# Kernel tuning notes

Hardware: AMD Instinct MI355X
Metric: run time of the kernel (lower is better)

Reference implementation:

```python
import jax, jax.numpy as jnp
import numpy as np

B, G, H, C = 2, 3072, 5, 2  # batch, genes (input_size), heads, classes
EPS = 1e-6


def setup_inputs() -> dict:
    key = jax.random.key(0)
    ks = jax.random.split(key, 11)
    xav = np.sqrt(2.0 / (G + 1)).astype(np.float32)  # xavier_normal for (G,1) slices
    inp = {"x": jax.random.normal(ks[0], (B, G), jnp.float32)}
    names = ["WQ1", "WK1", "WV1", "WQ2", "WK2", "WV2", "WQ3", "WK3", "WV3"]
    for i, name in enumerate(names):
        inp[name] = jax.random.normal(ks[1 + i], (H, G), jnp.float32) * xav
    inp["W0_1"] = jnp.full((H,), 0.001, jnp.float32)
    inp["W0_2"] = jnp.full((H,), 0.001, jnp.float32)
    inp["W0_3"] = jnp.full((H,), 0.001, jnp.float32)
    inp["ln_a"] = jnp.ones((G,), jnp.float32)
    inp["ln_b"] = jnp.zeros((G,), jnp.float32)
    inp["fc_w"] = jax.random.normal(ks[10], (C, G), jnp.float32) * np.sqrt(1.0 / G).astype(np.float32)
    inp["fc_b"] = jnp.zeros((C,), jnp.float32)
    return inp


def _multihead_attn(x, WQ, WK, WV, W0):
    # x: (B,G); WQ/WK/WV: (H,G); W0: (H,)
    # per head: scores[b,i,j] = (x[b,i]*WQ[h,i]) * (x[b,j]*WK[h,j])
    # z = softmax_j(scores); zero diagonal (mask AFTER softmax, no renorm);
    # out[b,i] = sum_j z[b,i,j] * (x[b,j]*WV[h,j])
    mask = 1.0 - jnp.eye(G, dtype=x.dtype)
    outs = []
    for h in range(H):  # small structural loop over heads (checkpointed loop in torch)
        q = x * WQ[h]                                   # (B,G)
        k = x * WK[h]                                   # (B,G)
        v = x * WV[h]                                   # (B,G)
        scores = q[:, :, None] * k[:, None, :]          # (B,G,G)
        z = jax.nn.softmax(scores, axis=2) * mask       # (B,G,G)
        outs.append(jnp.einsum('bij,bj->bi', z, v))     # (B,G)
    out_h = jnp.stack(outs, axis=-1)                    # (B,G,H)
    return jnp.einsum('bgh,h->bg', out_h, W0)


def _layernorm(x, a, b):
    # torch layernorm clone: unbiased std (ddof=1), eps added to std (not var)
    mean = jnp.mean(x, axis=-1, keepdims=True)
    std = jnp.std(x, axis=-1, keepdims=True, ddof=1)
    return a * (x - mean) / (std + EPS) + b


def reference(x, WQ1, WK1, WV1, WQ2, WK2, WV2, WQ3, WK3, WV3,
              W0_1, W0_2, W0_3, ln_a, ln_b, fc_w, fc_b):
    o1 = _multihead_attn(x, WQ1, WK1, WV1, W0_1)
    h1 = x + _layernorm(o1, ln_a, ln_b)      # res_connect (dropout=identity, eval)
    o2 = _multihead_attn(h1, WQ2, WK2, WV2, W0_2)
    h2 = h1 + _layernorm(o2, ln_a, ln_b)
    o3 = _multihead_attn(h2, WQ3, WK3, WV3, W0_3)
    h3 = h2 + _layernorm(o3, ln_a, ln_b)
    # act_fun='linear' -> identity; final classifier head
    return h3 @ fc_w.T + fc_b                # (B, C)
```

## Files before the change

kernel.cpp:

```cpp
#include <hip/hip_runtime.h>
#include <math.h>

typedef float v2f __attribute__((ext_vector_type(2)));

constexpr int Gn = 3072;
constexpr int Hn = 5;
constexpr float EPSf = 1e-6f;
constexpr float L2E  = 1.4426950408889634f;

__constant__ float INVFL[5] = {
  1.0f, 0.6931471805599453f, 0.2402265069591007f,
  0.05550410866482158f, 0.009618129107628477f };

struct __align__(16) Smem {
  float hbuf[Gn];
  float coeff[Hn * 16];
  float part[15][10];
  v2f   red2[16];
};

__device__ __forceinline__ v2f mk2(float a, float b){ v2f r; r.x = a; r.y = b; return r; }
__device__ __forceinline__ v2f pk_mul(v2f a, v2f b){
  v2f d; asm("v_pk_mul_f32 %0, %1, %2" : "=v"(d) : "v"(a), "v"(b)); return d; }
__device__ __forceinline__ v2f pk_add(v2f a, v2f b){
  v2f d; asm("v_pk_add_f32 %0, %1, %2" : "=v"(d) : "v"(a), "v"(b)); return d; }
__device__ __forceinline__ v2f pk_fma(v2f a, v2f b, v2f c){
  v2f d; asm("v_pk_fma_f32 %0, %1, %2, %3" : "=v"(d) : "v"(a), "v"(b), "v"(c)); return d; }

__device__ __forceinline__ float wave_red(float v) {
  int x;
  x = __builtin_amdgcn_update_dpp(0, __float_as_int(v), 0xB1,  0xF, 0xF, true);
  v += __int_as_float(x);
  x = __builtin_amdgcn_update_dpp(0, __float_as_int(v), 0x4E,  0xF, 0xF, true);
  v += __int_as_float(x);
  x = __builtin_amdgcn_update_dpp(0, __float_as_int(v), 0x141, 0xF, 0xF, true);
  v += __int_as_float(x);
  x = __builtin_amdgcn_update_dpp(0, __float_as_int(v), 0x140, 0xF, 0xF, true);
  v += __int_as_float(x);
  v += __shfl_xor(v, 16, 64);
  v += __shfl_xor(v, 32, 64);
  return v;
}

__device__ void layer(const float* __restrict__ WQ, const float* __restrict__ WK,
                      const float* __restrict__ WV, const float* __restrict__ W0,
                      const float* lnar, const float* lnbr, Smem& sm, int t)
{
  const int w = t >> 6, lane = t & 63;

  if (w < 15) {
    const int h = w / 3, sl = w % 3;
    const float4* xb4 = reinterpret_cast<const float4*>(sm.hbuf) + sl * 256;
    const float4* wk4 = reinterpret_cast<const float4*>(WK + h * Gn) + sl * 256;
    const float4* wv4 = reinterpret_cast<const float4*>(WV + h * Gn) + sl * 256;

    float4 xv[4], kk[4], vv[4];
#pragma unroll
    for (int it = 0; it < 4; ++it) {
      xv[it] = xb4[it * 64 + lane];
      kk[it] = wk4[it * 64 + lane];
      vv[it] = wv4[it * 64 + lane];
    }

    v2f N1 = mk2(0,0), N2 = N1, N3 = N1, N4 = N1;
    v2f M0 = N1, M1 = N1, M2 = N1, M3 = N1, M4 = N1;
    auto accp = [&](v2f x, v2f wkv, v2f wvv) {
      v2f k = pk_mul(x, wkv), v = pk_mul(x, wvv);
      v2f p2 = pk_mul(k, k), p3 = pk_mul(p2, k), p4 = pk_mul(p2, p2);
      N1 = pk_add(N1, k); N2 = pk_add(N2, p2); N3 = pk_add(N3, p3); N4 = pk_add(N4, p4);
      M0 = pk_add(M0, v);
      M1 = pk_fma(k,  v, M1); M2 = pk_fma(p2, v, M2);
      M3 = pk_fma(p3, v, M3); M4 = pk_fma(p4, v, M4);
    };
#pragma unroll
    for (int it = 0; it < 4; ++it) {
      accp(mk2(xv[it].x, xv[it].y), mk2(kk[it].x, kk[it].y), mk2(vv[it].x, vv[it].y));
      accp(mk2(xv[it].z, xv[it].w), mk2(kk[it].z, kk[it].w), mk2(vv[it].z, vv[it].w));
    }

    float r[9];
    r[0] = wave_red(N1.x + N1.y); r[1] = wave_red(N2.x + N2.y);
    r[2] = wave_red(N3.x + N3.y); r[3] = wave_red(N4.x + N4.y);
    r[4] = wave_red(M0.x + M0.y); r[5] = wave_red(M1.x + M1.y);
    r[6] = wave_red(M2.x + M2.y); r[7] = wave_red(M3.x + M3.y);
    r[8] = wave_red(M4.x + M4.y);
    if (lane == 0) {
#pragma unroll
      for (int m = 0; m < 9; ++m) sm.part[w][m] = r[m];
    }
  }
  __syncthreads();

  if (t < 45) {
    const int h = t / 9, r = t % 9;
    const float s = sm.part[h*3+0][r] + sm.part[h*3+1][r] + sm.part[h*3+2][r];
    const int m   = (r < 4) ? (r + 1) : (r - 4);
    const int dst = (r < 4) ? (r + 1) : (8 + (r - 4));
    sm.coeff[h*16 + dst] = s * INVFL[m];
  } else if (t < 50) {
    sm.coeff[(t - 45) * 16] = (float)Gn;
  }
  __syncthreads();

  const float xx0 = sm.hbuf[t], xx1 = sm.hbuf[t+1024], xx2 = sm.hbuf[t+2048];

  float w0r[Hn];
#pragma unroll
  for (int h = 0; h < Hn; ++h) w0r[h] = W0[h];

  float qc0,qc1,qc2, kc0,kc1,kc2, vc0,vc1,vc2;
  {
    const float* wq = WQ + t; const float* wk = WK + t; const float* wv = WV + t;
    qc0 = wq[0]; qc1 = wq[1024]; qc2 = wq[2048];
    kc0 = wk[0]; kc1 = wk[1024]; kc2 = wk[2048];
    vc0 = wv[0]; vc1 = wv[1024]; vc2 = wv[2048];
  }

  v2f o01 = mk2(0.f, 0.f);
  float o2a = 0.f;
#pragma unroll
  for (int h = 0; h < Hn; ++h) {
    float qn0,qn1,qn2, kn0,kn1,kn2, vn0,vn1,vn2;
    if (h < Hn - 1) {
      const float* wq = WQ + (h+1)*Gn + t;
      const float* wk = WK + (h+1)*Gn + t;
      const float* wv = WV + (h+1)*Gn + t;
      qn0 = wq[0]; qn1 = wq[1024]; qn2 = wq[2048];
      kn0 = wk[0]; kn1 = wk[1024]; kn2 = wk[2048];
      vn0 = wv[0]; vn1 = wv[1024]; vn2 = wv[2048];
    }
    const float4 zA = *reinterpret_cast<const float4*>(&sm.coeff[h*16]);
    const float  z4 = sm.coeff[h*16 + 4];
    const float4 fA = *reinterpret_cast<const float4*>(&sm.coeff[h*16 + 8]);
    const float  f4 = sm.coeff[h*16 + 12];
    const float  w0 = w0r[h];

    const v2f X  = mk2(xx0, xx1);
    const v2f qe = pk_mul(pk_mul(X, mk2(qc0, qc1)), mk2(L2E, L2E));
    const v2f kp = pk_mul(X, mk2(kc0, kc1));
    const v2f vp = pk_mul(X, mk2(vc0, vc1));
    v2f Z = mk2(z4, z4);
    Z = pk_fma(Z, qe, mk2(zA.w, zA.w)); Z = pk_fma(Z, qe, mk2(zA.z, zA.z));
    Z = pk_fma(Z, qe, mk2(zA.y, zA.y)); Z = pk_fma(Z, qe, mk2(zA.x, zA.x));
    v2f F = mk2(f4, f4);
    F = pk_fma(F, qe, mk2(fA.w, fA.w)); F = pk_fma(F, qe, mk2(fA.z, fA.z));
    F = pk_fma(F, qe, mk2(fA.y, fA.y)); F = pk_fma(F, qe, mk2(fA.x, fA.x));
    const v2f qk = pk_mul(qe, kp);
    const float Ex = __builtin_amdgcn_exp2f(qk.x), Ey = __builtin_amdgcn_exp2f(qk.y);
    const float rx = fmaf(-Ex, vp.x, F.x) * __builtin_amdgcn_rcpf(Z.x);
    const float ry = fmaf(-Ey, vp.y, F.y) * __builtin_amdgcn_rcpf(Z.y);
    o01 = pk_fma(mk2(w0, w0), mk2(rx, ry), o01);

    const float qe2 = xx2 * qc2 * L2E, k2 = xx2 * kc2, vv2 = xx2 * vc2;
    float Zs = z4;
    Zs = fmaf(Zs, qe2, zA.w); Zs = fmaf(Zs, qe2, zA.z);
    Zs = fmaf(Zs, qe2, zA.y); Zs = fmaf(Zs, qe2, zA.x);
    float Fs = f4;
    Fs = fmaf(Fs, qe2, fA.w); Fs = fmaf(Fs, qe2, fA.z);
    Fs = fmaf(Fs, qe2, fA.y); Fs = fmaf(Fs, qe2, fA.x);
    const float Es = __builtin_amdgcn_exp2f(qe2 * k2);
    o2a = fmaf(w0, fmaf(-Es, vv2, Fs) * __builtin_amdgcn_rcpf(Zs), o2a);

    if (h < Hn - 1) {
      qc0=qn0; qc1=qn1; qc2=qn2; kc0=kn0; kc1=kn1; kc2=kn2; vc0=vn0; vc1=vn1; vc2=vn2;
    }
  }

  float s1 = o01.x + o01.y + o2a;
  float s2 = fmaf(o01.x, o01.x, fmaf(o01.y, o01.y, o2a * o2a));
  s1 = wave_red(s1); s2 = wave_red(s2);
  if (lane == 0) sm.red2[w] = mk2(s1, s2);
  __syncthreads();
  v2f acc = sm.red2[0];
#pragma unroll
  for (int k = 1; k < 16; ++k) acc = pk_add(acc, sm.red2[k]);
  const float mean = acc.x * (1.f / (float)Gn);
  const float var  = fmaxf((acc.y - acc.x * mean) * (1.f / (float)(Gn - 1)), 0.f);
  const float inv  = __builtin_amdgcn_rcpf(sqrtf(var) + EPSf);
  sm.hbuf[t]      = xx0 + lnar[0] * (o01.x - mean) * inv + lnbr[0];
  sm.hbuf[t+1024] = xx1 + lnar[1] * (o01.y - mean) * inv + lnbr[1];
  sm.hbuf[t+2048] = xx2 + lnar[2] * (o2a   - mean) * inv + lnbr[2];
  __syncthreads();
}

__global__ __launch_bounds__(1024, 4) void net_kernel(
    const float* __restrict__ x,
    const float* __restrict__ WQ1, const float* __restrict__ WK1, const float* __restrict__ WV1,
    const float* __restrict__ WQ2, const float* __restrict__ WK2, const float* __restrict__ WV2,
    const float* __restrict__ WQ3, const float* __restrict__ WK3, const float* __restrict__ WV3,
    const float* __restrict__ W01, const float* __restrict__ W02, const float* __restrict__ W03,
    const float* __restrict__ lna, const float* __restrict__ lnb,
    const float* __restrict__ fcw, const float* __restrict__ fcb,
    float* __restrict__ out)
{
  __shared__ Smem sm;
  const int b = blockIdx.x;
  const int t = threadIdx.x;

  float lnar[3], lnbr[3];
#pragma unroll
  for (int rep = 0; rep < 3; ++rep) {
    const int i = rep * 1024 + t;
    sm.hbuf[i] = x[b * Gn + i];
    lnar[rep] = lna[i];
    lnbr[rep] = lnb[i];
  }
  __syncthreads();

  layer(WQ1, WK1, WV1, W01, lnar, lnbr, sm, t);
  layer(WQ2, WK2, WV2, W02, lnar, lnbr, sm, t);
  layer(WQ3, WK3, WV3, W03, lnar, lnbr, sm, t);

  v2f sacc = mk2(0.f, 0.f);
#pragma unroll
  for (int rep = 0; rep < 3; ++rep) {
    const int i = rep * 1024 + t;
    const float hv = sm.hbuf[i];
    sacc = pk_fma(mk2(hv, hv), mk2(fcw[i], fcw[Gn + i]), sacc);
  }
  const float s0 = wave_red(sacc.x), s1 = wave_red(sacc.y);
  const int w = t >> 6, lane = t & 63;
  if (lane == 0) sm.red2[w] = mk2(s0, s1);
  __syncthreads();
  if (t == 0) {
    v2f acc = sm.red2[0];
#pragma unroll
    for (int k = 1; k < 16; ++k) acc = pk_add(acc, sm.red2[k]);
    out[b * 2 + 0] = acc.x + fcb[0];
    out[b * 2 + 1] = acc.y + fcb[1];
  }
}

extern "C" void kernel_launch(void* const* d_in, const int* in_sizes, int n_in,
                              void* d_out, int out_size, void* d_ws, size_t ws_size,
                              hipStream_t stream) {
  const float* x    = (const float*)d_in[0];
  const float* WQ1  = (const float*)d_in[1];
  const float* WK1  = (const float*)d_in[2];
  const float* WV1  = (const float*)d_in[3];
  const float* WQ2  = (const float*)d_in[4];
  const float* WK2  = (const float*)d_in[5];
  const float* WV2  = (const float*)d_in[6];
  const float* WQ3  = (const float*)d_in[7];
  const float* WK3  = (const float*)d_in[8];
  const float* WV3  = (const float*)d_in[9];
  const float* W01  = (const float*)d_in[10];
  const float* W02  = (const float*)d_in[11];
  const float* W03  = (const float*)d_in[12];
  const float* ln_a = (const float*)d_in[13];
  const float* ln_b = (const float*)d_in[14];
  const float* fc_w = (const float*)d_in[15];
  const float* fc_b = (const float*)d_in[16];

  net_kernel<<<2, 1024, 0, stream>>>(x,
      WQ1, WK1, WV1, WQ2, WK2, WV2, WQ3, WK3, WV3,
      W01, W02, W03, ln_a, ln_b, fc_w, fc_b, (float*)d_out);
}
```

Baseline: 24.53 us.

## Split each batch row across four blocks with global-memory barriers between layers

Launches eight blocks instead of two, so each batch row's 3072 genes are split across four workgroups of 768 elements each. Per-layer moment sums and layernorm statistics are exchanged through workspace memory with release/acquire atomics and a token-based spin barrier. Each layer's weights are preloaded into registers before the barrier. This spreads the memory loads and compute over more CUs, at the cost of seven grid-wide barriers whose latency may outweigh the gain. Correctness relies on all eight blocks being co-resident and on the workspace token persisting across calls.

```diff
diff --git a/kernel.cpp b/kernel.cpp
--- a/kernel.cpp
+++ b/kernel.cpp
@@ -2,9 +2,13 @@
 #include <math.h>
 
 typedef float v2f __attribute__((ext_vector_type(2)));
+typedef unsigned long long u64;
 
 constexpr int Gn = 3072;
 constexpr int Hn = 5;
+constexpr int NQ = 4;
+constexpr int NBLK = 8;
+constexpr int QG = Gn / NQ;
 constexpr float EPSf = 1e-6f;
 constexpr float L2E  = 1.4426950408889634f;
 
@@ -12,14 +16,7 @@
   1.0f, 0.6931471805599453f, 0.2402265069591007f,
   0.05550410866482158f, 0.009618129107628477f };
 
-struct __align__(16) Smem {
-  float hbuf[Gn];
-  float coeff[Hn * 16];
-  float part[15][10];
-  v2f   red2[16];
-};
-
-__device__ __forceinline__ v2f mk2(float a, float b){ v2f r; r.x = a; r.y = b; return r; }
+__device__ __forceinline__ v2f mk2(float a, float b){ v2f r; r.x=a; r.y=b; return r; }
 __device__ __forceinline__ v2f pk_mul(v2f a, v2f b){
   v2f d; asm("v_pk_mul_f32 %0, %1, %2" : "=v"(d) : "v"(a), "v"(b)); return d; }
 __device__ __forceinline__ v2f pk_add(v2f a, v2f b){
@@ -42,144 +39,22 @@
   return v;
 }
 
-__device__ void layer(const float* __restrict__ WQ, const float* __restrict__ WK,
-                      const float* __restrict__ WV, const float* __restrict__ W0,
-                      const float* lnar, const float* lnbr, Smem& sm, int t)
-{
-  const int w = t >> 6, lane = t & 63;
-
-  if (w < 15) {
-    const int h = w / 3, sl = w % 3;
-    const float4* xb4 = reinterpret_cast<const float4*>(sm.hbuf) + sl * 256;
-    const float4* wk4 = reinterpret_cast<const float4*>(WK + h * Gn) + sl * 256;
-    const float4* wv4 = reinterpret_cast<const float4*>(WV + h * Gn) + sl * 256;
-
-    float4 xv[4], kk[4], vv[4];
-#pragma unroll
-    for (int it = 0; it < 4; ++it) {
-      xv[it] = xb4[it * 64 + lane];
-      kk[it] = wk4[it * 64 + lane];
-      vv[it] = wv4[it * 64 + lane];
-    }
-
-    v2f N1 = mk2(0,0), N2 = N1, N3 = N1, N4 = N1;
-    v2f M0 = N1, M1 = N1, M2 = N1, M3 = N1, M4 = N1;
-    auto accp = [&](v2f x, v2f wkv, v2f wvv) {
-      v2f k = pk_mul(x, wkv), v = pk_mul(x, wvv);
-      v2f p2 = pk_mul(k, k), p3 = pk_mul(p2, k), p4 = pk_mul(p2, p2);
-      N1 = pk_add(N1, k); N2 = pk_add(N2, p2); N3 = pk_add(N3, p3); N4 = pk_add(N4, p4);
-      M0 = pk_add(M0, v);
-      M1 = pk_fma(k,  v, M1); M2 = pk_fma(p2, v, M2);
-      M3 = pk_fma(p3, v, M3); M4 = pk_fma(p4, v, M4);
-    };
-#pragma unroll
-    for (int it = 0; it < 4; ++it) {
-      accp(mk2(xv[it].x, xv[it].y), mk2(kk[it].x, kk[it].y), mk2(vv[it].x, vv[it].y));
-      accp(mk2(xv[it].z, xv[it].w), mk2(kk[it].z, kk[it].w), mk2(vv[it].z, vv[it].w));
-    }
-
-    float r[9];
-    r[0] = wave_red(N1.x + N1.y); r[1] = wave_red(N2.x + N2.y);
-    r[2] = wave_red(N3.x + N3.y); r[3] = wave_red(N4.x + N4.y);
-    r[4] = wave_red(M0.x + M0.y); r[5] = wave_red(M1.x + M1.y);
-    r[6] = wave_red(M2.x + M2.y); r[7] = wave_red(M3.x + M3.y);
-    r[8] = wave_red(M4.x + M4.y);
-    if (lane == 0) {
-#pragma unroll
-      for (int m = 0; m < 9; ++m) sm.part[w][m] = r[m];
-    }
-  }
-  __syncthreads();
-
-  if (t < 45) {
-    const int h = t / 9, r = t % 9;
-    const float s = sm.part[h*3+0][r] + sm.part[h*3+1][r] + sm.part[h*3+2][r];
-    const int m   = (r < 4) ? (r + 1) : (r - 4);
-    const int dst = (r < 4) ? (r + 1) : (8 + (r - 4));
-    sm.coeff[h*16 + dst] = s * INVFL[m];
-  } else if (t < 50) {
-    sm.coeff[(t - 45) * 16] = (float)Gn;
-  }
-  __syncthreads();
-
-  const float xx0 = sm.hbuf[t], xx1 = sm.hbuf[t+1024], xx2 = sm.hbuf[t+2048];
-
-  float w0r[Hn];
-#pragma unroll
-  for (int h = 0; h < Hn; ++h) w0r[h] = W0[h];
-
-  float qc0,qc1,qc2, kc0,kc1,kc2, vc0,vc1,vc2;
-  {
-    const float* wq = WQ + t; const float* wk = WK + t; const float* wv = WV + t;
-    qc0 = wq[0]; qc1 = wq[1024]; qc2 = wq[2048];
-    kc0 = wk[0]; kc1 = wk[1024]; kc2 = wk[2048];
-    vc0 = wv[0]; vc1 = wv[1024]; vc2 = wv[2048];
-  }
-
-  v2f o01 = mk2(0.f, 0.f);
-  float o2a = 0.f;
-#pragma unroll
-  for (int h = 0; h < Hn; ++h) {
-    float qn0,qn1,qn2, kn0,kn1,kn2, vn0,vn1,vn2;
-    if (h < Hn - 1) {
-      const float* wq = WQ + (h+1)*Gn + t;
-      const float* wk = WK + (h+1)*Gn + t;
-      const float* wv = WV + (h+1)*Gn + t;
-      qn0 = wq[0]; qn1 = wq[1024]; qn2 = wq[2048];
-      kn0 = wk[0]; kn1 = wk[1024]; kn2 = wk[2048];
-      vn0 = wv[0]; vn1 = wv[1024]; vn2 = wv[2048];
-    }
-    const float4 zA = *reinterpret_cast<const float4*>(&sm.coeff[h*16]);
-    const float  z4 = sm.coeff[h*16 + 4];
-    const float4 fA = *reinterpret_cast<const float4*>(&sm.coeff[h*16 + 8]);
-    const float  f4 = sm.coeff[h*16 + 12];
-    const float  w0 = w0r[h];
-
-    const v2f X  = mk2(xx0, xx1);
-    const v2f qe = pk_mul(pk_mul(X, mk2(qc0, qc1)), mk2(L2E, L2E));
-    const v2f kp = pk_mul(X, mk2(kc0, kc1));
-    const v2f vp = pk_mul(X, mk2(vc0, vc1));
-    v2f Z = mk2(z4, z4);
-    Z = pk_fma(Z, qe, mk2(zA.w, zA.w)); Z = pk_fma(Z, qe, mk2(zA.z, zA.z));
-    Z = pk_fma(Z, qe, mk2(zA.y, zA.y)); Z = pk_fma(Z, qe, mk2(zA.x, zA.x));
-    v2f F = mk2(f4, f4);
-    F = pk_fma(F, qe, mk2(fA.w, fA.w)); F = pk_fma(F, qe, mk2(fA.z, fA.z));
-    F = pk_fma(F, qe, mk2(fA.y, fA.y)); F = pk_fma(F, qe, mk2(fA.x, fA.x));
-    const v2f qk = pk_mul(qe, kp);
-    const float Ex = __builtin_amdgcn_exp2f(qk.x), Ey = __builtin_amdgcn_exp2f(qk.y);
-    const float rx = fmaf(-Ex, vp.x, F.x) * __builtin_amdgcn_rcpf(Z.x);
-    const float ry = fmaf(-Ey, vp.y, F.y) * __builtin_amdgcn_rcpf(Z.y);
-    o01 = pk_fma(mk2(w0, w0), mk2(rx, ry), o01);
-
-    const float qe2 = xx2 * qc2 * L2E, k2 = xx2 * kc2, vv2 = xx2 * vc2;
-    float Zs = z4;
-    Zs = fmaf(Zs, qe2, zA.w); Zs = fmaf(Zs, qe2, zA.z);
-    Zs = fmaf(Zs, qe2, zA.y); Zs = fmaf(Zs, qe2, zA.x);
-    float Fs = f4;
-    Fs = fmaf(Fs, qe2, fA.w); Fs = fmaf(Fs, qe2, fA.z);
-    Fs = fmaf(Fs, qe2, fA.y); Fs = fmaf(Fs, qe2, fA.x);
-    const float Es = __builtin_amdgcn_exp2f(qe2 * k2);
-    o2a = fmaf(w0, fmaf(-Es, vv2, Fs) * __builtin_amdgcn_rcpf(Zs), o2a);
-
-    if (h < Hn - 1) {
-      qc0=qn0; qc1=qn1; qc2=qn2; kc0=kn0; kc1=kn1; kc2=kn2; vc0=vn0; vc1=vn1; vc2=vn2;
-    }
-  }
-
-  float s1 = o01.x + o01.y + o2a;
-  float s2 = fmaf(o01.x, o01.x, fmaf(o01.y, o01.y, o2a * o2a));
-  s1 = wave_red(s1); s2 = wave_red(s2);
-  if (lane == 0) sm.red2[w] = mk2(s1, s2);
-  __syncthreads();
-  v2f acc = sm.red2[0];
-#pragma unroll
-  for (int k = 1; k < 16; ++k) acc = pk_add(acc, sm.red2[k]);
-  const float mean = acc.x * (1.f / (float)Gn);
-  const float var  = fmaxf((acc.y - acc.x * mean) * (1.f / (float)(Gn - 1)), 0.f);
-  const float inv  = __builtin_amdgcn_rcpf(sqrtf(var) + EPSf);
-  sm.hbuf[t]      = xx0 + lnar[0] * (o01.x - mean) * inv + lnbr[0];
-  sm.hbuf[t+1024] = xx1 + lnar[1] * (o01.y - mean) * inv + lnbr[1];
-  sm.hbuf[t+2048] = xx2 + lnar[2] * (o2a   - mean) * inv + lnbr[2];
+__device__ __forceinline__ u64 pack2(float a, float b) {
+  return ((u64)__float_as_uint(b) << 32) | (u64)__float_as_uint(a);
+}
+
+__device__ __forceinline__ void gbar(u64* flags, int k, int blk, u64 tok, int t) {
+  __syncthreads();
+  if (t == 0) {
+    __threadfence();
+    __hip_atomic_store(&flags[(k * NBLK + blk) * 8], tok,
+                       __ATOMIC_RELEASE, __HIP_MEMORY_SCOPE_AGENT);
+  }
+  if (t < NBLK) {
+    while (__hip_atomic_load(&flags[(k * NBLK + t) * 8],
+                             __ATOMIC_ACQUIRE, __HIP_MEMORY_SCOPE_AGENT) != tok)
+      __builtin_amdgcn_s_sleep(1);
+  }
   __syncthreads();
 }
 
@@ -191,44 +66,208 @@
     const float* __restrict__ W01, const float* __restrict__ W02, const float* __restrict__ W03,
     const float* __restrict__ lna, const float* __restrict__ lnb,
     const float* __restrict__ fcw, const float* __restrict__ fcb,
-    float* __restrict__ out)
+    float* __restrict__ out, u64* __restrict__ wsu)
 {
-  __shared__ Smem sm;
-  const int b = blockIdx.x;
+  __shared__ float hbuf[QG];
+  __shared__ float coeff[Hn * 16];
+  __shared__ float part[15][9];
+  __shared__ v2f   red2[16];
+  __shared__ float lnsc[2];
+
   const int t = threadIdx.x;
-
-  float lnar[3], lnbr[3];
-#pragma unroll
-  for (int rep = 0; rep < 3; ++rep) {
-    const int i = rep * 1024 + t;
-    sm.hbuf[i] = x[b * Gn + i];
-    lnar[rep] = lna[i];
-    lnbr[rep] = lnb[i];
-  }
-  __syncthreads();
-
-  layer(WQ1, WK1, WV1, W01, lnar, lnbr, sm, t);
-  layer(WQ2, WK2, WV2, W02, lnar, lnbr, sm, t);
-  layer(WQ3, WK3, WV3, W03, lnar, lnbr, sm, t);
-
-  v2f sacc = mk2(0.f, 0.f);
-#pragma unroll
-  for (int rep = 0; rep < 3; ++rep) {
-    const int i = rep * 1024 + t;
-    const float hv = sm.hbuf[i];
-    sacc = pk_fma(mk2(hv, hv), mk2(fcw[i], fcw[Gn + i]), sacc);
-  }
-  const float s0 = wave_red(sacc.x), s1 = wave_red(sacc.y);
+  const int blk = blockIdx.x;
+  const int b = blk >> 2, q = blk & 3;
   const int w = t >> 6, lane = t & 63;
-  if (lane == 0) sm.red2[w] = mk2(s0, s1);
+
+  u64*   flags = wsu + 8;
+  float* mom   = (float*)(wsu + 8 + 7 * NBLK * 8);
+  u64*   lnst  = (u64*)(mom + 2 * NQ * 48);
+  u64*   fcst  = lnst + NBLK;
+
+  const u64 tok = __hip_atomic_load(wsu, __ATOMIC_ACQUIRE, __HIP_MEMORY_SCOPE_AGENT) + 1;
+
+  const float* WQs[3] = {WQ1, WQ2, WQ3};
+  const float* WKs[3] = {WK1, WK2, WK3};
+  const float* WVs[3] = {WV1, WV2, WV3};
+  const float* W0s[3] = {W01, W02, W03};
+
+  float hv = 0.f, ar = 0.f, br = 0.f;
+  if (t < QG) {
+    const int gi = q * QG + t;
+    hv = x[b * Gn + gi];
+    ar = lna[gi];
+    br = lnb[gi];
+    hbuf[t] = hv;
+  }
+  __syncthreads();
+
+#pragma unroll
+  for (int l = 0; l < 3; ++l) {
+    const float* WQ = WQs[l]; const float* WK = WKs[l];
+    const float* WV = WVs[l]; const float* W0 = W0s[l];
+
+    if (w < 15) {
+      const int h = w / 3, sub = w % 3;
+      const int jl = sub * 256 + lane * 4;
+      const float4 xv = *reinterpret_cast<const float4*>(&hbuf[jl]);
+      const float4 kk = *reinterpret_cast<const float4*>(&WK[h * Gn + q * QG + jl]);
+      const float4 vv = *reinterpret_cast<const float4*>(&WV[h * Gn + q * QG + jl]);
+
+      v2f N1 = mk2(0,0), N2 = N1, N3 = N1, N4 = N1;
+      v2f M0 = N1, M1 = N1, M2 = N1, M3 = N1, M4 = N1;
+      auto accp = [&](v2f xx, v2f wkv, v2f wvv) {
+        v2f k = pk_mul(xx, wkv), v = pk_mul(xx, wvv);
+        v2f p2 = pk_mul(k, k), p3 = pk_mul(p2, k), p4 = pk_mul(p2, p2);
+        N1 = pk_add(N1, k); N2 = pk_add(N2, p2); N3 = pk_add(N3, p3); N4 = pk_add(N4, p4);
+        M0 = pk_add(M0, v);
+        M1 = pk_fma(k,  v, M1); M2 = pk_fma(p2, v, M2);
+        M3 = pk_fma(p3, v, M3); M4 = pk_fma(p4, v, M4);
+      };
+      accp(mk2(xv.x, xv.y), mk2(kk.x, kk.y), mk2(vv.x, vv.y));
+      accp(mk2(xv.z, xv.w), mk2(kk.z, kk.w), mk2(vv.z, vv.w));
+
+      float r[9];
+      r[0] = wave_red(N1.x + N1.y); r[1] = wave_red(N2.x + N2.y);
+      r[2] = wave_red(N3.x + N3.y); r[3] = wave_red(N4.x + N4.y);
+      r[4] = wave_red(M0.x + M0.y); r[5] = wave_red(M1.x + M1.y);
+      r[6] = wave_red(M2.x + M2.y); r[7] = wave_red(M3.x + M3.y);
+      r[8] = wave_red(M4.x + M4.y);
+      if (lane == 0) {
+#pragma unroll
+        for (int m = 0; m < 9; ++m) part[w][m] = r[m];
+      }
+    }
+
+    float w0r[Hn], pq[Hn], pkw[Hn], pvw[Hn];
+#pragma unroll
+    for (int h = 0; h < Hn; ++h) w0r[h] = W0[h];
+    if (t < QG) {
+      const int gi = q * QG + t;
+#pragma unroll
+      for (int h = 0; h < Hn; ++h) {
+        pq[h]  = WQ[h * Gn + gi];
+        pkw[h] = WK[h * Gn + gi];
+        pvw[h] = WV[h * Gn + gi];
+        asm volatile("" : "+v"(pq[h]), "+v"(pkw[h]), "+v"(pvw[h]));
+      }
+    }
+
+    __syncthreads();
+    if (t < 45) {
+      const int h = t / 9, r = t % 9;
+      const float s = part[h*3+0][r] + part[h*3+1][r] + part[h*3+2][r];
+      __hip_atomic_store(&mom[(b * NQ + q) * 48 + t], s,
+                         __ATOMIC_RELEASE, __HIP_MEMORY_SCOPE_AGENT);
+    }
+
+    gbar(flags, 2 * l, blk, tok, t);
+
+    if (t < 45) {
+      float s = 0.f;
+#pragma unroll
+      for (int qq = 0; qq < NQ; ++qq)
+        s += __hip_atomic_load(&mom[(b * NQ + qq) * 48 + t],
+                               __ATOMIC_ACQUIRE, __HIP_MEMORY_SCOPE_AGENT);
+      const int h = t / 9, r = t % 9;
+      const int m   = (r < 4) ? (r + 1) : (r - 4);
+      const int dst = (r < 4) ? (r + 1) : (8 + (r - 4));
+      coeff[h * 16 + dst] = s * INVFL[m];
+    } else if (t < 50) {
+      coeff[(t - 45) * 16] = (float)Gn;
+    }
+    __syncthreads();
+
+    float o = 0.f;
+    if (t < QG) {
+#pragma unroll
+      for (int h = 0; h < Hn; ++h) {
+        const float4 zA = *reinterpret_cast<const float4*>(&coeff[h * 16]);
+        const float  z4 = coeff[h * 16 + 4];
+        const float4 fA = *reinterpret_cast<const float4*>(&coeff[h * 16 + 8]);
+        const float  f4 = coeff[h * 16 + 12];
+        const float qe = hv * pq[h] * L2E;
+        const float kf = hv * pkw[h];
+        const float vf = hv * pvw[h];
+        float Z = z4;
+        Z = fmaf(Z, qe, zA.w); Z = fmaf(Z, qe, zA.z);
+        Z = fmaf(Z, qe, zA.y); Z = fmaf(Z, qe, zA.x);
+        float F = f4;
+        F = fmaf(F, qe, fA.w); F = fmaf(F, qe, fA.z);
+        F = fmaf(F, qe, fA.y); F = fmaf(F, qe, fA.x);
+        const float E = __builtin_amdgcn_exp2f(qe * kf);
+        o = fmaf(w0r[h], fmaf(-E, vf, F) * __builtin_amdgcn_rcpf(Z), o);
+      }
+    }
+
+    float s1 = wave_red(o);
+    float s2 = wave_red(o * o);
+    if (lane == 0) red2[w] = mk2(s1, s2);
+    __syncthreads();
+    if (t == 0) {
+      v2f acc = red2[0];
+#pragma unroll
+      for (int k = 1; k < 16; ++k) acc = pk_add(acc, red2[k]);
+      __hip_atomic_store(&lnst[b * NQ + q], pack2(acc.x, acc.y),
+                         __ATOMIC_RELEASE, __HIP_MEMORY_SCOPE_AGENT);
+    }
+
+    gbar(flags, 2 * l + 1, blk, tok, t);
+
+    if (t == 0) {
+      float a = 0.f, ss = 0.f;
+#pragma unroll
+      for (int qq = 0; qq < NQ; ++qq) {
+        const u64 p = __hip_atomic_load(&lnst[b * NQ + qq],
+                                        __ATOMIC_ACQUIRE, __HIP_MEMORY_SCOPE_AGENT);
+        a  += __uint_as_float((unsigned)(p & 0xffffffffu));
+        ss += __uint_as_float((unsigned)(p >> 32));
+      }
+      const float mean = a * (1.f / (float)Gn);
+      const float var  = fmaxf((ss - a * mean) * (1.f / (float)(Gn - 1)), 0.f);
+      lnsc[0] = mean;
+      lnsc[1] = __builtin_amdgcn_rcpf(sqrtf(var) + EPSf);
+    }
+    __syncthreads();
+    if (t < QG) {
+      hv = hv + ar * (o - lnsc[0]) * lnsc[1] + br;
+      hbuf[t] = hv;
+    }
+    __syncthreads();
+  }
+
+  float s0 = 0.f, s1 = 0.f;
+  if (t < QG) {
+    const int gi = q * QG + t;
+    s0 = hv * fcw[gi];
+    s1 = hv * fcw[Gn + gi];
+  }
+  s0 = wave_red(s0); s1 = wave_red(s1);
+  if (lane == 0) red2[w] = mk2(s0, s1);
   __syncthreads();
   if (t == 0) {
-    v2f acc = sm.red2[0];
-#pragma unroll
-    for (int k = 1; k < 16; ++k) acc = pk_add(acc, sm.red2[k]);
-    out[b * 2 + 0] = acc.x + fcb[0];
-    out[b * 2 + 1] = acc.y + fcb[1];
-  }
+    v2f acc = red2[0];
+#pragma unroll
+    for (int k = 1; k < 16; ++k) acc = pk_add(acc, red2[k]);
+    __hip_atomic_store(&fcst[b * NQ + q], pack2(acc.x, acc.y),
+                       __ATOMIC_RELEASE, __HIP_MEMORY_SCOPE_AGENT);
+  }
+
+  gbar(flags, 6, blk, tok, t);
+
+  if (q == 0 && t == 0) {
+    float a0 = 0.f, a1 = 0.f;
+#pragma unroll
+    for (int qq = 0; qq < NQ; ++qq) {
+      const u64 p = __hip_atomic_load(&fcst[b * NQ + qq],
+                                      __ATOMIC_ACQUIRE, __HIP_MEMORY_SCOPE_AGENT);
+      a0 += __uint_as_float((unsigned)(p & 0xffffffffu));
+      a1 += __uint_as_float((unsigned)(p >> 32));
+    }
+    out[b * 2 + 0] = a0 + fcb[0];
+    out[b * 2 + 1] = a1 + fcb[1];
+  }
+  if (blk == 0 && t == 0)
+    __hip_atomic_store(wsu, tok, __ATOMIC_RELEASE, __HIP_MEMORY_SCOPE_AGENT);
 }
 
 extern "C" void kernel_launch(void* const* d_in, const int* in_sizes, int n_in,
@@ -252,7 +291,8 @@
   const float* fc_w = (const float*)d_in[15];
   const float* fc_b = (const float*)d_in[16];
 
-  net_kernel<<<2, 1024, 0, stream>>>(x,
+  net_kernel<<<NBLK, 1024, 0, stream>>>(x,
       WQ1, WK1, WV1, WQ2, WK2, WV2, WQ3, WK3, WV3,
-      W01, W02, W03, ln_a, ln_b, fc_w, fc_b, (float*)d_out);
-}
+      W01, W02, W03, ln_a, ln_b, fc_w, fc_b,
+      (float*)d_out, (u64*)d_ws);
+}
```

After: 35.15 us. +43.3%, slower.

## Inline layers, keep state in registers, prefetch all head weights before reduction

Applied to the files above, without the earlier changes.

The layer function is inlined into a three-iteration loop. The hidden state, layernorm params and fc weights now stay in registers instead of being re-read from shared memory. All five heads' Q/K/V weights are loaded up front, before the wave reductions and barriers, so global latency overlaps the moment reduction instead of being prefetched one head at a time. The final barrier is dropped on the last layer, a separate reduction buffer avoids a race, and a tree sum replaces the serial 16-way sum. The trade-off is higher register pressure from holding 45 weight values per thread.

```diff
diff --git a/kernel.cpp b/kernel.cpp
--- a/kernel.cpp
+++ b/kernel.cpp
@@ -15,11 +15,12 @@
 struct __align__(16) Smem {
   float hbuf[Gn];
   float coeff[Hn * 16];
-  float part[15][10];
+  float part[15][9];
   v2f   red2[16];
+  v2f   red2b[16];
 };
 
-__device__ __forceinline__ v2f mk2(float a, float b){ v2f r; r.x = a; r.y = b; return r; }
+__device__ __forceinline__ v2f mk2(float a, float b){ v2f r; r.x=a; r.y=b; return r; }
 __device__ __forceinline__ v2f pk_mul(v2f a, v2f b){
   v2f d; asm("v_pk_mul_f32 %0, %1, %2" : "=v"(d) : "v"(a), "v"(b)); return d; }
 __device__ __forceinline__ v2f pk_add(v2f a, v2f b){
@@ -42,145 +43,14 @@
   return v;
 }
 
-__device__ void layer(const float* __restrict__ WQ, const float* __restrict__ WK,
-                      const float* __restrict__ WV, const float* __restrict__ W0,
-                      const float* lnar, const float* lnbr, Smem& sm, int t)
-{
-  const int w = t >> 6, lane = t & 63;
-
-  if (w < 15) {
-    const int h = w / 3, sl = w % 3;
-    const float4* xb4 = reinterpret_cast<const float4*>(sm.hbuf) + sl * 256;
-    const float4* wk4 = reinterpret_cast<const float4*>(WK + h * Gn) + sl * 256;
-    const float4* wv4 = reinterpret_cast<const float4*>(WV + h * Gn) + sl * 256;
-
-    float4 xv[4], kk[4], vv[4];
-#pragma unroll
-    for (int it = 0; it < 4; ++it) {
-      xv[it] = xb4[it * 64 + lane];
-      kk[it] = wk4[it * 64 + lane];
-      vv[it] = wv4[it * 64 + lane];
-    }
-
-    v2f N1 = mk2(0,0), N2 = N1, N3 = N1, N4 = N1;
-    v2f M0 = N1, M1 = N1, M2 = N1, M3 = N1, M4 = N1;
-    auto accp = [&](v2f x, v2f wkv, v2f wvv) {
-      v2f k = pk_mul(x, wkv), v = pk_mul(x, wvv);
-      v2f p2 = pk_mul(k, k), p3 = pk_mul(p2, k), p4 = pk_mul(p2, p2);
-      N1 = pk_add(N1, k); N2 = pk_add(N2, p2); N3 = pk_add(N3, p3); N4 = pk_add(N4, p4);
-      M0 = pk_add(M0, v);
-      M1 = pk_fma(k,  v, M1); M2 = pk_fma(p2, v, M2);
-      M3 = pk_fma(p3, v, M3); M4 = pk_fma(p4, v, M4);
-    };
-#pragma unroll
-    for (int it = 0; it < 4; ++it) {
-      accp(mk2(xv[it].x, xv[it].y), mk2(kk[it].x, kk[it].y), mk2(vv[it].x, vv[it].y));
-      accp(mk2(xv[it].z, xv[it].w), mk2(kk[it].z, kk[it].w), mk2(vv[it].z, vv[it].w));
-    }
-
-    float r[9];
-    r[0] = wave_red(N1.x + N1.y); r[1] = wave_red(N2.x + N2.y);
-    r[2] = wave_red(N3.x + N3.y); r[3] = wave_red(N4.x + N4.y);
-    r[4] = wave_red(M0.x + M0.y); r[5] = wave_red(M1.x + M1.y);
-    r[6] = wave_red(M2.x + M2.y); r[7] = wave_red(M3.x + M3.y);
-    r[8] = wave_red(M4.x + M4.y);
-    if (lane == 0) {
-#pragma unroll
-      for (int m = 0; m < 9; ++m) sm.part[w][m] = r[m];
-    }
-  }
-  __syncthreads();
-
-  if (t < 45) {
-    const int h = t / 9, r = t % 9;
-    const float s = sm.part[h*3+0][r] + sm.part[h*3+1][r] + sm.part[h*3+2][r];
-    const int m   = (r < 4) ? (r + 1) : (r - 4);
-    const int dst = (r < 4) ? (r + 1) : (8 + (r - 4));
-    sm.coeff[h*16 + dst] = s * INVFL[m];
-  } else if (t < 50) {
-    sm.coeff[(t - 45) * 16] = (float)Gn;
-  }
-  __syncthreads();
-
-  const float xx0 = sm.hbuf[t], xx1 = sm.hbuf[t+1024], xx2 = sm.hbuf[t+2048];
-
-  float w0r[Hn];
-#pragma unroll
-  for (int h = 0; h < Hn; ++h) w0r[h] = W0[h];
-
-  float qc0,qc1,qc2, kc0,kc1,kc2, vc0,vc1,vc2;
-  {
-    const float* wq = WQ + t; const float* wk = WK + t; const float* wv = WV + t;
-    qc0 = wq[0]; qc1 = wq[1024]; qc2 = wq[2048];
-    kc0 = wk[0]; kc1 = wk[1024]; kc2 = wk[2048];
-    vc0 = wv[0]; vc1 = wv[1024]; vc2 = wv[2048];
-  }
-
-  v2f o01 = mk2(0.f, 0.f);
-  float o2a = 0.f;
-#pragma unroll
-  for (int h = 0; h < Hn; ++h) {
-    float qn0,qn1,qn2, kn0,kn1,kn2, vn0,vn1,vn2;
-    if (h < Hn - 1) {
-      const float* wq = WQ + (h+1)*Gn + t;
-      const float* wk = WK + (h+1)*Gn + t;
-      const float* wv = WV + (h+1)*Gn + t;
-      qn0 = wq[0]; qn1 = wq[1024]; qn2 = wq[2048];
-      kn0 = wk[0]; kn1 = wk[1024]; kn2 = wk[2048];
-      vn0 = wv[0]; vn1 = wv[1024]; vn2 = wv[2048];
-    }
-    const float4 zA = *reinterpret_cast<const float4*>(&sm.coeff[h*16]);
-    const float  z4 = sm.coeff[h*16 + 4];
-    const float4 fA = *reinterpret_cast<const float4*>(&sm.coeff[h*16 + 8]);
-    const float  f4 = sm.coeff[h*16 + 12];
-    const float  w0 = w0r[h];
-
-    const v2f X  = mk2(xx0, xx1);
-    const v2f qe = pk_mul(pk_mul(X, mk2(qc0, qc1)), mk2(L2E, L2E));
-    const v2f kp = pk_mul(X, mk2(kc0, kc1));
-    const v2f vp = pk_mul(X, mk2(vc0, vc1));
-    v2f Z = mk2(z4, z4);
-    Z = pk_fma(Z, qe, mk2(zA.w, zA.w)); Z = pk_fma(Z, qe, mk2(zA.z, zA.z));
-    Z = pk_fma(Z, qe, mk2(zA.y, zA.y)); Z = pk_fma(Z, qe, mk2(zA.x, zA.x));
-    v2f F = mk2(f4, f4);
-    F = pk_fma(F, qe, mk2(fA.w, fA.w)); F = pk_fma(F, qe, mk2(fA.z, fA.z));
-    F = pk_fma(F, qe, mk2(fA.y, fA.y)); F = pk_fma(F, qe, mk2(fA.x, fA.x));
-    const v2f qk = pk_mul(qe, kp);
-    const float Ex = __builtin_amdgcn_exp2f(qk.x), Ey = __builtin_amdgcn_exp2f(qk.y);
-    const float rx = fmaf(-Ex, vp.x, F.x) * __builtin_amdgcn_rcpf(Z.x);
-    const float ry = fmaf(-Ey, vp.y, F.y) * __builtin_amdgcn_rcpf(Z.y);
-    o01 = pk_fma(mk2(w0, w0), mk2(rx, ry), o01);
-
-    const float qe2 = xx2 * qc2 * L2E, k2 = xx2 * kc2, vv2 = xx2 * vc2;
-    float Zs = z4;
-    Zs = fmaf(Zs, qe2, zA.w); Zs = fmaf(Zs, qe2, zA.z);
-    Zs = fmaf(Zs, qe2, zA.y); Zs = fmaf(Zs, qe2, zA.x);
-    float Fs = f4;
-    Fs = fmaf(Fs, qe2, fA.w); Fs = fmaf(Fs, qe2, fA.z);
-    Fs = fmaf(Fs, qe2, fA.y); Fs = fmaf(Fs, qe2, fA.x);
-    const float Es = __builtin_amdgcn_exp2f(qe2 * k2);
-    o2a = fmaf(w0, fmaf(-Es, vv2, Fs) * __builtin_amdgcn_rcpf(Zs), o2a);
-
-    if (h < Hn - 1) {
-      qc0=qn0; qc1=qn1; qc2=qn2; kc0=kn0; kc1=kn1; kc2=kn2; vc0=vn0; vc1=vn1; vc2=vn2;
-    }
-  }
-
-  float s1 = o01.x + o01.y + o2a;
-  float s2 = fmaf(o01.x, o01.x, fmaf(o01.y, o01.y, o2a * o2a));
-  s1 = wave_red(s1); s2 = wave_red(s2);
-  if (lane == 0) sm.red2[w] = mk2(s1, s2);
-  __syncthreads();
-  v2f acc = sm.red2[0];
-#pragma unroll
-  for (int k = 1; k < 16; ++k) acc = pk_add(acc, sm.red2[k]);
-  const float mean = acc.x * (1.f / (float)Gn);
-  const float var  = fmaxf((acc.y - acc.x * mean) * (1.f / (float)(Gn - 1)), 0.f);
-  const float inv  = __builtin_amdgcn_rcpf(sqrtf(var) + EPSf);
-  sm.hbuf[t]      = xx0 + lnar[0] * (o01.x - mean) * inv + lnbr[0];
-  sm.hbuf[t+1024] = xx1 + lnar[1] * (o01.y - mean) * inv + lnbr[1];
-  sm.hbuf[t+2048] = xx2 + lnar[2] * (o2a   - mean) * inv + lnbr[2];
-  __syncthreads();
+__device__ __forceinline__ v2f tree16(const v2f* r) {
+  v2f a0 = pk_add(r[0], r[8]),  a1 = pk_add(r[1], r[9]);
+  v2f a2 = pk_add(r[2], r[10]), a3 = pk_add(r[3], r[11]);
+  v2f a4 = pk_add(r[4], r[12]), a5 = pk_add(r[5], r[13]);
+  v2f a6 = pk_add(r[6], r[14]), a7 = pk_add(r[7], r[15]);
+  a0 = pk_add(a0, a4); a1 = pk_add(a1, a5); a2 = pk_add(a2, a6); a3 = pk_add(a3, a7);
+  a0 = pk_add(a0, a2); a1 = pk_add(a1, a3);
+  return pk_add(a0, a1);
 }
 
 __global__ __launch_bounds__(1024, 4) void net_kernel(
@@ -196,38 +66,166 @@
   __shared__ Smem sm;
   const int b = blockIdx.x;
   const int t = threadIdx.x;
-
-  float lnar[3], lnbr[3];
-#pragma unroll
-  for (int rep = 0; rep < 3; ++rep) {
-    const int i = rep * 1024 + t;
-    sm.hbuf[i] = x[b * Gn + i];
-    lnar[rep] = lna[i];
-    lnbr[rep] = lnb[i];
+  const int w = t >> 6, lane = t & 63;
+
+  const float* WQs[3] = {WQ1, WQ2, WQ3};
+  const float* WKs[3] = {WK1, WK2, WK3};
+  const float* WVs[3] = {WV1, WV2, WV3};
+  const float* W0s[3] = {W01, W02, W03};
+
+  float xx0 = x[b*Gn + t], xx1 = x[b*Gn + t + 1024], xx2 = x[b*Gn + t + 2048];
+  const float la0 = lna[t], la1 = lna[t+1024], la2 = lna[t+2048];
+  const float lb0 = lnb[t], lb1 = lnb[t+1024], lb2 = lnb[t+2048];
+  const float fw00 = fcw[t],      fw01 = fcw[t+1024],      fw02 = fcw[t+2048];
+  const float fw10 = fcw[Gn + t], fw11 = fcw[Gn + t+1024], fw12 = fcw[Gn + t+2048];
+  sm.hbuf[t] = xx0; sm.hbuf[t+1024] = xx1; sm.hbuf[t+2048] = xx2;
+  __syncthreads();
+
+#pragma unroll
+  for (int l = 0; l < 3; ++l) {
+    const float* WQ = WQs[l]; const float* WK = WKs[l];
+    const float* WV = WVs[l]; const float* W0 = W0s[l];
+
+    v2f N1 = mk2(0,0), N2 = N1, N3 = N1, N4 = N1;
+    v2f M0 = N1, M1 = N1, M2 = N1, M3 = N1, M4 = N1;
+    if (w < 15) {
+      const int h = w / 3, sl = w % 3;
+      const float4* xb4 = reinterpret_cast<const float4*>(sm.hbuf) + sl * 256;
+      const float4* wk4 = reinterpret_cast<const float4*>(WK + h * Gn) + sl * 256;
+      const float4* wv4 = reinterpret_cast<const float4*>(WV + h * Gn) + sl * 256;
+      float4 xv[4], kk[4], vv[4];
+#pragma unroll
+      for (int it = 0; it < 4; ++it) {
+        xv[it] = xb4[it * 64 + lane];
+        kk[it] = wk4[it * 64 + lane];
+        vv[it] = wv4[it * 64 + lane];
+      }
+      auto accp = [&](v2f xx, v2f wkv, v2f wvv) {
+        v2f k = pk_mul(xx, wkv), v = pk_mul(xx, wvv);
+        v2f p2 = pk_mul(k, k), p3 = pk_mul(p2, k), p4 = pk_mul(p2, p2);
+        N1 = pk_add(N1, k); N2 = pk_add(N2, p2); N3 = pk_add(N3, p3); N4 = pk_add(N4, p4);
+        M0 = pk_add(M0, v);
+        M1 = pk_fma(k,  v, M1); M2 = pk_fma(p2, v, M2);
+        M3 = pk_fma(p3, v, M3); M4 = pk_fma(p4, v, M4);
+      };
+#pragma unroll
+      for (int it = 0; it < 4; ++it) {
+        accp(mk2(xv[it].x, xv[it].y), mk2(kk[it].x, kk[it].y), mk2(vv[it].x, vv[it].y));
+        accp(mk2(xv[it].z, xv[it].w), mk2(kk[it].z, kk[it].w), mk2(vv[it].z, vv[it].w));
+      }
+    }
+
+    float pqA[Hn], pkA[Hn], pvA[Hn];
+    float pqB[Hn], pkB[Hn], pvB[Hn];
+    float pqC[Hn], pkC[Hn], pvC[Hn];
+#pragma unroll
+    for (int h = 0; h < Hn; ++h) {
+      const float* wq = WQ + h * Gn + t;
+      const float* wk = WK + h * Gn + t;
+      const float* wv = WV + h * Gn + t;
+      pqA[h] = wq[0]; pqB[h] = wq[1024]; pqC[h] = wq[2048];
+      pkA[h] = wk[0]; pkB[h] = wk[1024]; pkC[h] = wk[2048];
+      pvA[h] = wv[0]; pvB[h] = wv[1024]; pvC[h] = wv[2048];
+    }
+    float w0r[Hn];
+#pragma unroll
+    for (int h = 0; h < Hn; ++h) w0r[h] = W0[h];
+
+    if (w < 15) {
+      float r[9];
+      r[0] = wave_red(N1.x + N1.y); r[1] = wave_red(N2.x + N2.y);
+      r[2] = wave_red(N3.x + N3.y); r[3] = wave_red(N4.x + N4.y);
+      r[4] = wave_red(M0.x + M0.y); r[5] = wave_red(M1.x + M1.y);
+      r[6] = wave_red(M2.x + M2.y); r[7] = wave_red(M3.x + M3.y);
+      r[8] = wave_red(M4.x + M4.y);
+      if (lane == 0) {
+#pragma unroll
+        for (int m = 0; m < 9; ++m) sm.part[w][m] = r[m];
+      }
+    }
+    __syncthreads();
+
+    if (t < 45) {
+      const int h = t / 9, r = t % 9;
+      const float s = sm.part[h*3+0][r] + sm.part[h*3+1][r] + sm.part[h*3+2][r];
+      const int m   = (r < 4) ? (r + 1) : (r - 4);
+      const int dst = (r < 4) ? (r + 1) : (8 + (r - 4));
+      sm.coeff[h*16 + dst] = s * INVFL[m];
+    } else if (t < 50) {
+      sm.coeff[(t - 45) * 16] = (float)Gn;
+    }
+    __syncthreads();
+
+    v2f o01 = mk2(0.f, 0.f);
+    float o2a = 0.f;
+#pragma unroll
+    for (int h = 0; h < Hn; ++h) {
+      const float4 zA = *reinterpret_cast<const float4*>(&sm.coeff[h*16]);
+      const float  z4 = sm.coeff[h*16 + 4];
+      const float4 fA = *reinterpret_cast<const float4*>(&sm.coeff[h*16 + 8]);
+      const float  f4 = sm.coeff[h*16 + 12];
+      const float  w0 = w0r[h];
+
+      const v2f X  = mk2(xx0, xx1);
+      const v2f qe = pk_mul(pk_mul(X, mk2(pqA[h], pqB[h])), mk2(L2E, L2E));
+      const v2f kp = pk_mul(X, mk2(pkA[h], pkB[h]));
+      const v2f vp = pk_mul(X, mk2(pvA[h], pvB[h]));
+      v2f Z = mk2(z4, z4);
+      Z = pk_fma(Z, qe, mk2(zA.w, zA.w)); Z = pk_fma(Z, qe, mk2(zA.z, zA.z));
+      Z = pk_fma(Z, qe, mk2(zA.y, zA.y)); Z = pk_fma(Z, qe, mk2(zA.x, zA.x));
+      v2f F = mk2(f4, f4);
+      F = pk_fma(F, qe, mk2(fA.w, fA.w)); F = pk_fma(F, qe, mk2(fA.z, fA.z));
+      F = pk_fma(F, qe, mk2(fA.y, fA.y)); F = pk_fma(F, qe, mk2(fA.x, fA.x));
+      const v2f qk = pk_mul(qe, kp);
+      const float Ex = __builtin_amdgcn_exp2f(qk.x), Ey = __builtin_amdgcn_exp2f(qk.y);
+      const float rx = fmaf(-Ex, vp.x, F.x) * __builtin_amdgcn_rcpf(Z.x);
+      const float ry = fmaf(-Ey, vp.y, F.y) * __builtin_amdgcn_rcpf(Z.y);
+      o01 = pk_fma(mk2(w0, w0), mk2(rx, ry), o01);
+
+      const float qe2 = xx2 * pqC[h] * L2E;
+      const float k2  = xx2 * pkC[h];
+      const float v2  = xx2 * pvC[h];
+      float Zs = z4;
+      Zs = fmaf(Zs, qe2, zA.w); Zs = fmaf(Zs, qe2, zA.z);
+      Zs = fmaf(Zs, qe2, zA.y); Zs = fmaf(Zs, qe2, zA.x);
+      float Fs = f4;
+      Fs = fmaf(Fs, qe2, fA.w); Fs = fmaf(Fs, qe2, fA.z);
+      Fs = fmaf(Fs, qe2, fA.y); Fs = fmaf(Fs, qe2, fA.x);
+      const float Es = __builtin_amdgcn_exp2f(qe2 * k2);
+      o2a = fmaf(w0, fmaf(-Es, v2, Fs) * __builtin_amdgcn_rcpf(Zs), o2a);
+    }
+
+    float s1 = o01.x + o01.y + o2a;
+    float s2 = fmaf(o01.x, o01.x, fmaf(o01.y, o01.y, o2a * o2a));
+    s1 = wave_red(s1); s2 = wave_red(s2);
+    if (lane == 0) sm.red2[w] = mk2(s1, s2);
+    __syncthreads();
+    const v2f acc = tree16(sm.red2);
+    const float mean = acc.x * (1.f / (float)Gn);
+    const float var  = fmaxf((acc.y - acc.x * mean) * (1.f / (float)(Gn - 1)), 0.f);
+    const float inv  = __builtin_amdgcn_rcpf(sqrtf(var) + EPSf);
+    xx0 = xx0 + la0 * (o01.x - mean) * inv + lb0;
+    xx1 = xx1 + la1 * (o01.y - mean) * inv + lb1;
+    xx2 = xx2 + la2 * (o2a   - mean) * inv + lb2;
+    if (l < 2) {
+      sm.hbuf[t]      = xx0;
+      sm.hbuf[t+1024] = xx1;
+      sm.hbuf[t+2048] = xx2;
+      __syncthreads();
+    }
   }
-  __syncthreads();
-
-  layer(WQ1, WK1, WV1, W01, lnar, lnbr, sm, t);
-  layer(WQ2, WK2, WV2, W02, lnar, lnbr, sm, t);
-  layer(WQ3, WK3, WV3, W03, lnar, lnbr, sm, t);
 
   v2f sacc = mk2(0.f, 0.f);
-#pragma unroll
-  for (int rep = 0; rep < 3; ++rep) {
-    const int i = rep * 1024 + t;
-    const float hv = sm.hbuf[i];
-    sacc = pk_fma(mk2(hv, hv), mk2(fcw[i], fcw[Gn + i]), sacc);
-  }
+  sacc = pk_fma(mk2(xx0, xx0), mk2(fw00, fw10), sacc);
+  sacc = pk_fma(mk2(xx1, xx1), mk2(fw01, fw11), sacc);
+  sacc = pk_fma(mk2(xx2, xx2), mk2(fw02, fw12), sacc);
   const float s0 = wave_red(sacc.x), s1 = wave_red(sacc.y);
-  const int w = t >> 6, lane = t & 63;
-  if (lane == 0) sm.red2[w] = mk2(s0, s1);
+  if (lane == 0) sm.red2b[w] = mk2(s0, s1);
   __syncthreads();
   if (t == 0) {
-    v2f acc = sm.red2[0];
-#pragma unroll
-    for (int k = 1; k < 16; ++k) acc = pk_add(acc, sm.red2[k]);
-    out[b * 2 + 0] = acc.x + fcb[0];
-    out[b * 2 + 1] = acc.y + fcb[1];
+    const v2f acc = tree16(sm.red2b);
+    out[b*2 + 0] = acc.x + fcb[0];
+    out[b*2 + 1] = acc.y + fcb[1];
   }
 }
 
```

New measurement: 25.65 us. 4.6% more time.
